# Optimization experiments

Measured on AMD Instinct MI355X. Metric: run time of the kernel, lower is better.

Reference implementation:

```python
import jax, jax.numpy as jnp
import numpy as np

N_NODES = 50000
N_EDGES = 800000
N_GRAPHS = 512
NEG_SLOPE = 0.2  # PyG GATv2Conv default negative_slope

# layer dims: (in_feat, out_channels, heads)
LAYER_DIMS = [(11, 64, 3), (192, 64, 3), (192, 64, 3), (192, 20, 1)]


def setup_inputs() -> dict:
    key = jax.random.key(0)
    ks = jax.random.split(key, 4 + 6 * len(LAYER_DIMS))
    inp = {}
    inp["x"] = jax.random.normal(ks[0], (N_NODES, 11), jnp.float32)
    src = jax.random.randint(ks[1], (N_EDGES,), 0, N_NODES, dtype=jnp.int32)
    dst = jax.random.randint(ks[2], (N_EDGES,), 0, N_NODES, dtype=jnp.int32)
    inp["edge_index"] = jnp.stack([src, dst])
    inp["batch"] = jnp.sort(jax.random.randint(ks[3], (N_NODES,), 0, N_GRAPHS, dtype=jnp.int32))
    ki = 4
    for li, (fi, ch, h) in enumerate(LAYER_DIMS):
        fo = h * ch
        s = 1.0 / np.sqrt(fi)
        inp[f"Wl{li}"] = jax.random.normal(ks[ki + 0], (fo, fi), jnp.float32) * s
        inp[f"bl{li}"] = jnp.zeros((fo,), jnp.float32)
        inp[f"Wr{li}"] = jax.random.normal(ks[ki + 1], (fo, fi), jnp.float32) * s
        inp[f"br{li}"] = jnp.zeros((fo,), jnp.float32)
        inp[f"att{li}"] = jax.random.normal(ks[ki + 2], (h, ch), jnp.float32) * (1.0 / np.sqrt(ch))
        inp[f"b{li}"] = jnp.zeros((fo,), jnp.float32)
        ki += 6
    return inp


def gatv2_layer(x, src, dst, Wl, bl, Wr, br, att, bias, heads, ch):
    """PyG GATv2Conv (concat=True): e = att . leaky_relu(lin_l(x_j)+lin_r(x_i)),
    alpha = softmax over incoming edges of each dst node, out = sum alpha * lin_l(x_j)."""
    N = x.shape[0]
    xl = (x @ Wl.T + bl).reshape(N, heads, ch)  # source transform [N,H,C]
    xr = (x @ Wr.T + br).reshape(N, heads, ch)  # target transform [N,H,C]
    m = xl[src] + xr[dst]                        # [E,H,C] edge-wise gather
    e = jnp.einsum("ehc,hc->eh", jax.nn.leaky_relu(m, NEG_SLOPE), att)  # [E,H]
    emax = jax.ops.segment_max(e, dst, num_segments=N)   # per-dst softmax (stable)
    p = jnp.exp(e - emax[dst])
    denom = jax.ops.segment_sum(p, dst, num_segments=N)
    alpha = p / denom[dst]                        # [E,H]
    out = jax.ops.segment_sum(xl[src] * alpha[..., None], dst, num_segments=N)
    return out.reshape(N, heads * ch) + bias


def reference(x, edge_index, batch,
              Wl0, bl0, Wr0, br0, att0, b0,
              Wl1, bl1, Wr1, br1, att1, b1,
              Wl2, bl2, Wr2, br2, att2, b2,
              Wl3, bl3, Wr3, br3, att3, b3):
    N = x.shape[0]
    loop = jnp.arange(N, dtype=edge_index.dtype)  # add_self_loops=True
    src = jnp.concatenate([edge_index[0], loop])
    dst = jnp.concatenate([edge_index[1], loop])
    h = gatv2_layer(x, src, dst, Wl0, bl0, Wr0, br0, att0, b0, 3, 64)
    h = jax.nn.relu(h)
    h = gatv2_layer(h, src, dst, Wl1, bl1, Wr1, br1, att1, b1, 3, 64)
    h = jax.nn.relu(h)
    h = gatv2_layer(h, src, dst, Wl2, bl2, Wr2, br2, att2, b2, 3, 64)
    h = jax.nn.relu(h)
    h = gatv2_layer(h, src, dst, Wl3, bl3, Wr3, br3, att3, b3, 1, 20)
    # global_add_pool
    return jax.ops.segment_sum(h, batch, num_segments=N_GRAPHS)  # [G, 20]
```

## Files before the change

### kernel.cpp

```cpp
#include <hip/hip_runtime.h>

#define NN 50000
#define NE 800000
#define NT 850000
#define NG 512

typedef __attribute__((ext_vector_type(8))) short bf16x8;
typedef __attribute__((ext_vector_type(4))) float f32x4;


template <int CTRL>
__device__ __forceinline__ float dpp_add(float x) {
  int y = __builtin_amdgcn_update_dpp(0, __float_as_int(x), CTRL, 0xF, 0xF, true);
  return x + __int_as_float(y);
}
template <int CTRL>
__device__ __forceinline__ float dpp_max(float x) {
  int y = __builtin_amdgcn_update_dpp(0, __float_as_int(x), CTRL, 0xF, 0xF, true);
  return fmaxf(x, __int_as_float(y));
}

__device__ __forceinline__ float swz16(float x) {
  return __int_as_float(__builtin_amdgcn_ds_swizzle(__float_as_int(x), 0x401F));
}

__device__ __forceinline__ float rowsum16(float x) {
  x = dpp_add<0xB1>(x);
  x = dpp_add<0x4E>(x);
  x = dpp_add<0x124>(x);
  x = dpp_add<0x128>(x);
  return x;
}
__device__ __forceinline__ float quadsum4(float x) {
  x = dpp_add<0xB1>(x);
  x = dpp_add<0x4E>(x);
  return x;
}
__device__ __forceinline__ float xg_sum(float x) {
  x += swz16(x);
  auto p = __builtin_amdgcn_permlane32_swap(__float_as_uint(x), __float_as_uint(x), false, false);
  return __uint_as_float(p[0]) + __uint_as_float(p[1]);
}
__device__ __forceinline__ float xg_max(float x) {
  x = fmaxf(x, swz16(x));
  auto p = __builtin_amdgcn_permlane32_swap(__float_as_uint(x), __float_as_uint(x), false, false);
  return fmaxf(__uint_as_float(p[0]), __uint_as_float(p[1]));
}
__device__ __forceinline__ float xq_sum(float x) {
  x = dpp_add<0x124>(x);
  x = dpp_add<0x128>(x);
  return xg_sum(x);
}
__device__ __forceinline__ float xq_max(float x) {
  x = dpp_max<0x124>(x);
  x = dpp_max<0x128>(x);
  return xg_max(x);
}

__device__ __forceinline__ float exp2_fast(float x) {
#if __has_builtin(__builtin_amdgcn_exp2f)
  return __builtin_amdgcn_exp2f(x);
#else
  return exp2f(x);
#endif
}

__device__ __forceinline__ float lrelu(float t) { return fmaxf(t, 0.2f * t); }

__device__ __forceinline__ unsigned int f2bf(float f) {
  unsigned int u = __float_as_uint(f);
  u = (u + 0x7FFFu + ((u >> 16) & 1u)) >> 16;
  return u;
}
__device__ __forceinline__ float bf_lo(unsigned int u) { return __uint_as_float(u << 16); }
__device__ __forceinline__ float bf_hi(unsigned int u) { return __uint_as_float(u & 0xFFFF0000u); }
__device__ __forceinline__ float4 bf2f4(uint2 u) {
  return make_float4(bf_lo(u.x), bf_hi(u.x), bf_lo(u.y), bf_hi(u.y));
}

__device__ __forceinline__ void pk_l(float2& d, float2 a, float2 b) {
  asm("v_pk_fma_f32 %0, %1, %2, %0 op_sel_hi:[0,1,1]" : "+v"(d) : "v"(a), "v"(b));
}
__device__ __forceinline__ void pk_h(float2& d, float2 a, float2 b) {
  asm("v_pk_fma_f32 %0, %1, %2, %0 op_sel:[1,0,0]" : "+v"(d) : "v"(a), "v"(b));
}


__global__ void k_hist(const int* __restrict__ dst, int* __restrict__ cnt) {
  int i = blockIdx.x * blockDim.x + threadIdx.x;
  if (i < NT) {
    int d = (i < NE) ? dst[i] : (i - NE);
    atomicAdd(&cnt[d], 1);
  }
}

__global__ __launch_bounds__(1024)
void k_scan(const int* __restrict__ cnt, int* __restrict__ offs) {
  __shared__ int sh[1024];
  int tid = threadIdx.x;
  const int CH = (NN + 1023) / 1024;
  int base = tid * CH;
  int s = 0;
  for (int i = 0; i < CH; ++i) {
    int idx = base + i;
    if (idx < NN) s += cnt[idx];
  }
  sh[tid] = s;
  __syncthreads();
  for (int off = 1; off < 1024; off <<= 1) {
    int t = (tid >= off) ? sh[tid - off] : 0;
    __syncthreads();
    sh[tid] += t;
    __syncthreads();
  }
  int prefix = (tid > 0) ? sh[tid - 1] : 0;
  for (int i = 0; i < CH; ++i) {
    int idx = base + i;
    if (idx < NN) {
      offs[idx] = prefix;
      prefix += cnt[idx];
    }
  }
  if (tid == 1023) offs[NN] = sh[1023];
}

__global__ void k_scatter(const int* __restrict__ src, const int* __restrict__ dst,
                          const int* __restrict__ offs, int* __restrict__ cur,
                          int* __restrict__ srt) {
  int i = blockIdx.x * blockDim.x + threadIdx.x;
  if (i < NT) {
    int s, d;
    if (i < NE) { s = src[i]; d = dst[i]; }
    else        { s = d = i - NE; }
    int pos = offs[d] + atomicAdd(&cur[d], 1);
    srt[pos] = s;
  }
}


__global__ void k_cvtW(const float* __restrict__ a, const float* __restrict__ b,
                       const float* __restrict__ c, const float* __restrict__ d,
                       const float* __restrict__ e, const float* __restrict__ f,
                       unsigned short* __restrict__ out) {
  int i = blockIdx.x * 256 + threadIdx.x;
  if (i >= 155136) return;
  float v;
  if      (i < 36864)  v = a[i];
  else if (i < 73728)  v = b[i - 36864];
  else if (i < 110592) v = c[i - 73728];
  else if (i < 147456) v = d[i - 110592];
  else if (i < 151296) v = e[i - 147456];
  else                 v = f[i - 151296];
  out[i] = (unsigned short)f2bf(v);
}


#define LSTR 200

__global__ __launch_bounds__(256)
void k_gemm_mfma2(const unsigned short* __restrict__ Abf,
                  const unsigned short* __restrict__ W1bf,
                  const unsigned short* __restrict__ W2bf,
                  const float* __restrict__ bias1, const float* __restrict__ bias2,
                  unsigned short* __restrict__ C1, unsigned short* __restrict__ C2,
                  int M, int FO) {
  __shared__ unsigned short Al[64 * LSTR];
  __shared__ unsigned short Bl[2][64 * LSTR];
  int tid = threadIdx.x;
  int mb = blockIdx.x * 64;
  int nb = blockIdx.y * 64;

  {
    int r = tid >> 2, q = tid & 3;
    int ga = min(mb + r, M - 1);
    int gb = min(nb + r, FO - 1);
    const unsigned short* pA = Abf  + (size_t)ga * 192 + q * 48;
    const unsigned short* p1 = W1bf + (size_t)gb * 192 + q * 48;
    const unsigned short* p2 = W2bf + (size_t)gb * 192 + q * 48;
    unsigned short* lA = Al + r * LSTR + q * 48;
    unsigned short* l1 = Bl[0] + r * LSTR + q * 48;
    unsigned short* l2 = Bl[1] + r * LSTR + q * 48;
#pragma unroll
    for (int i = 0; i < 6; ++i) {
      *(bf16x8*)(lA + i * 8) = *(const bf16x8*)(pA + i * 8);
      *(bf16x8*)(l1 + i * 8) = *(const bf16x8*)(p1 + i * 8);
      *(bf16x8*)(l2 + i * 8) = *(const bf16x8*)(p2 + i * 8);
    }
  }
  __syncthreads();

  int l = tid & 63, wid = tid >> 6;
  int wr = (wid >> 1) * 32, wc = (wid & 1) * 32;
  int lr = l & 15, lk = (l >> 4) * 8;

  f32x4 acc[2][2][2];
#pragma unroll
  for (int a = 0; a < 2; ++a)
#pragma unroll
    for (int b = 0; b < 2; ++b)
#pragma unroll
      for (int c = 0; c < 2; ++c) acc[a][b][c] = (f32x4){0.f, 0.f, 0.f, 0.f};

  const unsigned short* pa0 = Al + (wr + 0 + lr) * LSTR + lk;
  const unsigned short* pa1 = Al + (wr + 16 + lr) * LSTR + lk;
  const unsigned short* p10 = Bl[0] + (wc + 0 + lr) * LSTR + lk;
  const unsigned short* p11 = Bl[0] + (wc + 16 + lr) * LSTR + lk;
  const unsigned short* p20 = Bl[1] + (wc + 0 + lr) * LSTR + lk;
  const unsigned short* p21 = Bl[1] + (wc + 16 + lr) * LSTR + lk;
#pragma unroll
  for (int kt = 0; kt < 6; ++kt) {
    bf16x8 a0 = *(const bf16x8*)(pa0 + kt * 32);
    bf16x8 a1 = *(const bf16x8*)(pa1 + kt * 32);
    bf16x8 b10 = *(const bf16x8*)(p10 + kt * 32);
    bf16x8 b11 = *(const bf16x8*)(p11 + kt * 32);
    bf16x8 b20 = *(const bf16x8*)(p20 + kt * 32);
    bf16x8 b21 = *(const bf16x8*)(p21 + kt * 32);
    acc[0][0][0] = __builtin_amdgcn_mfma_f32_16x16x32_bf16(a0, b10, acc[0][0][0], 0, 0, 0);
    acc[0][0][1] = __builtin_amdgcn_mfma_f32_16x16x32_bf16(a0, b11, acc[0][0][1], 0, 0, 0);
    acc[0][1][0] = __builtin_amdgcn_mfma_f32_16x16x32_bf16(a1, b10, acc[0][1][0], 0, 0, 0);
    acc[0][1][1] = __builtin_amdgcn_mfma_f32_16x16x32_bf16(a1, b11, acc[0][1][1], 0, 0, 0);
    acc[1][0][0] = __builtin_amdgcn_mfma_f32_16x16x32_bf16(a0, b20, acc[1][0][0], 0, 0, 0);
    acc[1][0][1] = __builtin_amdgcn_mfma_f32_16x16x32_bf16(a0, b21, acc[1][0][1], 0, 0, 0);
    acc[1][1][0] = __builtin_amdgcn_mfma_f32_16x16x32_bf16(a1, b20, acc[1][1][0], 0, 0, 0);
    acc[1][1][1] = __builtin_amdgcn_mfma_f32_16x16x32_bf16(a1, b21, acc[1][1][1], 0, 0, 0);
  }

  int rb = (l >> 4) * 4;
#pragma unroll
  for (int mt = 0; mt < 2; ++mt) {
    unsigned short* C = mt == 0 ? C1 : C2;
    const float* bias = mt == 0 ? bias1 : bias2;
#pragma unroll
    for (int fn = 0; fn < 2; ++fn) {
      int col = nb + wc + fn * 16 + lr;
      if (col >= FO) continue;
      float bv = bias[col];
#pragma unroll
      for (int fm = 0; fm < 2; ++fm) {
        const f32x4& av = acc[mt][fm][fn];
#pragma unroll
        for (int i = 0; i < 4; ++i) {
          int row = mb + wr + fm * 16 + rb + i;
          if (row < M) C[(size_t)row * FO + col] = (unsigned short)f2bf(av[i] + bv);
        }
      }
    }
  }
}


__global__ __launch_bounds__(256)
void k_gemm_dual(const float* __restrict__ A, int M, int K, int FO,
                 const float* __restrict__ W1, const float* __restrict__ bias1,
                 const float* __restrict__ W2, const float* __restrict__ bias2,
                 unsigned short* __restrict__ C1, unsigned short* __restrict__ C2) {
  constexpr int CT = 16;
  constexpr int BN = CT * 4;
  constexpr int BR = (256 / CT) * 8;
  constexpr int AF4 = BR / 64;
  __shared__ float As[16][BR + 4];
  __shared__ float Bs[2][16][BN + 4];

  int tid = threadIdx.x;
  int tx = tid % CT, ty = tid / CT;
  int mb = blockIdx.x * BR, nb = blockIdx.y * BN;
  int nkt = (K + 15) >> 4;

  float4 sa[AF4], sb1, sb2;

  auto ldrow = [&](const float* P, int row, int lim, int k0, int kq) -> float4 {
    float4 v = make_float4(0.f, 0.f, 0.f, 0.f);
    if (row < lim) {
      float t[4];
#pragma unroll
      for (int i = 0; i < 4; ++i)
        t[i] = (k0 + kq + i < K) ? P[(size_t)row * K + k0 + kq + i] : 0.f;
      v = make_float4(t[0], t[1], t[2], t[3]);
    }
    return v;
  };

  auto loadg = [&](int kt) {
    int k0 = kt * 16;
#pragma unroll
    for (int q = 0; q < AF4; ++q) {
      int f4 = q * 256 + tid;
      sa[q] = ldrow(A, mb + (f4 >> 2), M, k0, (f4 & 3) * 4);
    }
    int row = tid >> 2, kq = (tid & 3) * 4;
    sb1 = ldrow(W1, nb + row, FO, k0, kq);
    sb2 = ldrow(W2, nb + row, FO, k0, kq);
  };

  auto stlds = [&]() {
#pragma unroll
    for (int q = 0; q < AF4; ++q) {
      int f4 = q * 256 + tid;
      int row = f4 >> 2, kq = (f4 & 3) * 4;
      As[kq + 0][row] = sa[q].x; As[kq + 1][row] = sa[q].y;
      As[kq + 2][row] = sa[q].z; As[kq + 3][row] = sa[q].w;
    }
    int row = tid >> 2, kq = (tid & 3) * 4;
    Bs[0][kq + 0][row] = sb1.x; Bs[0][kq + 1][row] = sb1.y;
    Bs[0][kq + 2][row] = sb1.z; Bs[0][kq + 3][row] = sb1.w;
    Bs[1][kq + 0][row] = sb2.x; Bs[1][kq + 1][row] = sb2.y;
    Bs[1][kq + 2][row] = sb2.z; Bs[1][kq + 3][row] = sb2.w;
  };

  float2 c1[8][2], c2[8][2];
#pragma unroll
  for (int r = 0; r < 8; ++r)
#pragma unroll
    for (int j = 0; j < 2; ++j) {
      c1[r][j] = make_float2(0.f, 0.f);
      c2[r][j] = make_float2(0.f, 0.f);
    }

  loadg(0);
  stlds();
  __syncthreads();

  for (int t = 0;;) {
#pragma unroll
    for (int k = 0; k < 16; ++k) {
      float4 av0 = *(const float4*)&As[k][ty * 8 + 0];
      float4 av1 = *(const float4*)&As[k][ty * 8 + 4];
      float4 bv1 = *(const float4*)&Bs[0][k][tx * 4];
      float4 bv2 = *(const float4*)&Bs[1][k][tx * 4];
      float2 f1a = make_float2(bv1.x, bv1.y), f1b = make_float2(bv1.z, bv1.w);
      float2 f2a = make_float2(bv2.x, bv2.y), f2b = make_float2(bv2.z, bv2.w);
      float2 a01 = make_float2(av0.x, av0.y), a23 = make_float2(av0.z, av0.w);
      float2 a45 = make_float2(av1.x, av1.y), a67 = make_float2(av1.z, av1.w);
#define PKROW(rp, a)                                                       \
      pk_l(c1[2 * rp + 0][0], a, f1a); pk_l(c1[2 * rp + 0][1], a, f1b);    \
      pk_h(c1[2 * rp + 1][0], a, f1a); pk_h(c1[2 * rp + 1][1], a, f1b);    \
      pk_l(c2[2 * rp + 0][0], a, f2a); pk_l(c2[2 * rp + 0][1], a, f2b);    \
      pk_h(c2[2 * rp + 1][0], a, f2a); pk_h(c2[2 * rp + 1][1], a, f2b);
      PKROW(0, a01) PKROW(1, a23) PKROW(2, a45) PKROW(3, a67)
#undef PKROW
    }
    if (++t == nkt) break;
    loadg(t);
    __syncthreads();
    stlds();
    __syncthreads();
  }

  int col = nb + tx * 4;
  if (col < FO) {
    float4 bb1 = *(const float4*)&bias1[col];
    float4 bb2 = *(const float4*)&bias2[col];
#pragma unroll
    for (int r = 0; r < 8; ++r) {
      int m = mb + ty * 8 + r;
      if (m >= M) continue;
      uint2 o1, o2;
      o1.x = f2bf(c1[r][0].x + bb1.x) | (f2bf(c1[r][0].y + bb1.y) << 16);
      o1.y = f2bf(c1[r][1].x + bb1.z) | (f2bf(c1[r][1].y + bb1.w) << 16);
      o2.x = f2bf(c2[r][0].x + bb2.x) | (f2bf(c2[r][0].y + bb2.y) << 16);
      o2.y = f2bf(c2[r][1].x + bb2.z) | (f2bf(c2[r][1].y + bb2.w) << 16);
      *(uint2*)&C1[(size_t)m * FO + col] = o1;
      *(uint2*)&C2[(size_t)m * FO + col] = o2;
    }
  }
}


__global__ __launch_bounds__(64)
void k_gat3(const unsigned short* __restrict__ xl, const unsigned short* __restrict__ xr,
            const float* __restrict__ att, const float* __restrict__ bias,
            const int* __restrict__ offs, const int* __restrict__ srt,
            unsigned short* __restrict__ obf, int relu) {
  const float L2E = 1.4426950408889634f;
  int lane = threadIdx.x;
  int grp = lane >> 4, lg = lane & 15;
  int n = blockIdx.x;

  float4 xrv[3], atv[3];
#pragma unroll
  for (int h = 0; h < 3; ++h) {
    xrv[h] = bf2f4(*(const uint2*)(xr + (size_t)n * 192 + h * 64 + lg * 4));
    float4 a = *(const float4*)&att[h * 64 + lg * 4];
    atv[h] = make_float4(a.x * L2E, a.y * L2E, a.z * L2E, a.w * L2E);
  }
  float m[3] = {-1e30f, -1e30f, -1e30f}, d[3] = {0.f, 0.f, 0.f};
  float4 acc[3];
#pragma unroll
  for (int h = 0; h < 3; ++h) acc[h] = make_float4(0.f, 0.f, 0.f, 0.f);

  int e0 = offs[n], e1 = offs[n + 1];
  int nch = (e1 - e0 + 3) >> 2;

  uint2 Rc[3];
  bool vc;
  int j = e0 + grp;
  {
    int jj = min(j, e1 - 1);
    int s = srt[jj];
    const unsigned short* b = xl + (size_t)s * 192 + lg * 4;
    Rc[0] = *(const uint2*)(b);
    Rc[1] = *(const uint2*)(b + 64);
    Rc[2] = *(const uint2*)(b + 128);
    vc = j < e1;
  }
  for (int it = 0; it < nch; ++it) {
    uint2 Rn[3];
    bool vn = false;
    int jn = j + 4;
    if (it + 1 < nch) {
      int jj = min(jn, e1 - 1);
      int s = srt[jj];
      const unsigned short* b = xl + (size_t)s * 192 + lg * 4;
      Rn[0] = *(const uint2*)(b);
      Rn[1] = *(const uint2*)(b + 64);
      Rn[2] = *(const uint2*)(b + 128);
      vn = jn < e1;
    }
    float4 Xc[3];
    Xc[0] = bf2f4(Rc[0]); Xc[1] = bf2f4(Rc[1]); Xc[2] = bf2f4(Rc[2]);
    float part[3];
#pragma unroll
    for (int h = 0; h < 3; ++h) {
      float t = lrelu(Xc[h].x + xrv[h].x);
      float pa = t * atv[h].x;
      t = lrelu(Xc[h].y + xrv[h].y); pa = fmaf(t, atv[h].y, pa);
      t = lrelu(Xc[h].z + xrv[h].z); pa = fmaf(t, atv[h].z, pa);
      t = lrelu(Xc[h].w + xrv[h].w); pa = fmaf(t, atv[h].w, pa);
      part[h] = pa;
    }
#pragma unroll
    for (int h = 0; h < 3; ++h) {
      part[h] = rowsum16(part[h]);
      part[h] = vc ? part[h] : -1e30f;
    }
    float g = fmaxf(fmaxf(part[0] - m[0], part[1] - m[1]), part[2] - m[2]);
    if (__any(g > 11.0f)) {
#pragma unroll
      for (int h = 0; h < 3; ++h) {
        float nm = fmaxf(m[h], part[h]);
        float sc = exp2_fast(m[h] - nm);
        d[h] *= sc;
        acc[h].x *= sc; acc[h].y *= sc; acc[h].z *= sc; acc[h].w *= sc;
        m[h] = nm;
      }
    }
#pragma unroll
    for (int h = 0; h < 3; ++h) {
      float p = vc ? exp2_fast(part[h] - m[h]) : 0.f;
      d[h] += p;
      acc[h].x = fmaf(p, Xc[h].x, acc[h].x);
      acc[h].y = fmaf(p, Xc[h].y, acc[h].y);
      acc[h].z = fmaf(p, Xc[h].z, acc[h].z);
      acc[h].w = fmaf(p, Xc[h].w, acc[h].w);
    }
    Rc[0] = Rn[0]; Rc[1] = Rn[1]; Rc[2] = Rn[2];
    vc = vn; j = jn;
  }

#pragma unroll
  for (int h = 0; h < 3; ++h) {
    float nm = xg_max(m[h]);
    float sc = exp2_fast(m[h] - nm);
    float D = xg_sum(d[h] * sc);
    float A0 = xg_sum(acc[h].x * sc);
    float A1 = xg_sum(acc[h].y * sc);
    float A2 = xg_sum(acc[h].z * sc);
    float A3 = xg_sum(acc[h].w * sc);
    if (grp == 0) {
      float4 bb = *(const float4*)&bias[h * 64 + lg * 4];
      float inv = 1.0f / D;
      float v0 = fmaf(A0, inv, bb.x);
      float v1 = fmaf(A1, inv, bb.y);
      float v2 = fmaf(A2, inv, bb.z);
      float v3 = fmaf(A3, inv, bb.w);
      if (relu) {
        v0 = fmaxf(v0, 0.f); v1 = fmaxf(v1, 0.f);
        v2 = fmaxf(v2, 0.f); v3 = fmaxf(v3, 0.f);
      }
      unsigned int lo = f2bf(v0) | (f2bf(v1) << 16);
      unsigned int hi = f2bf(v2) | (f2bf(v3) << 16);
      *(uint2*)(obf + (size_t)n * 192 + h * 64 + lg * 4) = make_uint2(lo, hi);
    }
  }
}


__global__ __launch_bounds__(64)
void k_gat1(const unsigned short* __restrict__ xl, const unsigned short* __restrict__ xr,
            const float* __restrict__ att, const float* __restrict__ bias,
            const int* __restrict__ offs, const int* __restrict__ srt,
            const int* __restrict__ batch, float* __restrict__ gout) {
  const float L2E = 1.4426950408889634f;
  int lane = threadIdx.x;
  int grp = lane >> 2, lg = lane & 3;
  int n = blockIdx.x;

  float xrv[5], atv[5];
#pragma unroll
  for (int i = 0; i < 5; ++i) {
    xrv[i] = bf_lo(xr[(size_t)n * 20 + lg * 5 + i]);
    atv[i] = att[lg * 5 + i] * L2E;
  }
  float m = -1e30f, d = 0.f, a[5] = {0.f, 0.f, 0.f, 0.f, 0.f};

  int e0 = offs[n], e1 = offs[n + 1];
  int nch = (e1 - e0 + 15) >> 4;

  float Xc[5];
  bool vc;
  int j = e0 + grp;
  {
    int jj = min(j, e1 - 1);
    int s = srt[jj];
    const unsigned short* b = xl + (size_t)s * 20 + lg * 5;
#pragma unroll
    for (int i = 0; i < 5; ++i) Xc[i] = bf_lo(b[i]);
    vc = j < e1;
  }
  for (int it = 0; it < nch; ++it) {
    float Xn[5] = {0.f, 0.f, 0.f, 0.f, 0.f};
    bool vn = false;
    int jn = j + 16;
    if (it + 1 < nch) {
      int jj = min(jn, e1 - 1);
      int s = srt[jj];
      const unsigned short* b = xl + (size_t)s * 20 + lg * 5;
#pragma unroll
      for (int i = 0; i < 5; ++i) Xn[i] = bf_lo(b[i]);
      vn = jn < e1;
    }
    float pa = lrelu(Xc[0] + xrv[0]) * atv[0];
#pragma unroll
    for (int i = 1; i < 5; ++i) pa = fmaf(lrelu(Xc[i] + xrv[i]), atv[i], pa);
    pa = quadsum4(pa);
    pa = vc ? pa : -1e30f;
    if (__any(pa - m > 11.0f)) {
      float nm = fmaxf(m, pa);
      float sc = exp2_fast(m - nm);
      d *= sc;
#pragma unroll
      for (int i = 0; i < 5; ++i) a[i] *= sc;
      m = nm;
    }
    float p = vc ? exp2_fast(pa - m) : 0.f;
    d += p;
#pragma unroll
    for (int i = 0; i < 5; ++i) a[i] = fmaf(p, Xc[i], a[i]);
#pragma unroll
    for (int i = 0; i < 5; ++i) Xc[i] = Xn[i];
    vc = vn; j = jn;
  }

  float nm = xq_max(m);
  float sc = exp2_fast(m - nm);
  float D = xq_sum(d * sc);
  float A[5];
#pragma unroll
  for (int i = 0; i < 5; ++i) A[i] = xq_sum(a[i] * sc);
  if (grp == 0) {
    int gb = batch[n] * 20 + lg * 5;
    float inv = 1.0f / D;
#pragma unroll
    for (int i = 0; i < 5; ++i)
      atomicAdd(&gout[gb + i], fmaf(A[i], inv, bias[lg * 5 + i]));
  }
}


extern "C" void kernel_launch(void* const* d_in, const int* in_sizes, int n_in,
                              void* d_out, int out_size, void* d_ws, size_t ws_size,
                              hipStream_t stream) {
  const float* x = (const float*)d_in[0];
  const int* src = (const int*)d_in[1];
  const int* dst = src + NE;
  const int* batch = (const int*)d_in[2];
  const float *Wl[4], *bl[4], *Wr[4], *br[4], *att[4], *bb[4];
  for (int li = 0; li < 4; ++li) {
    Wl[li]  = (const float*)d_in[3 + li * 6 + 0];
    bl[li]  = (const float*)d_in[3 + li * 6 + 1];
    Wr[li]  = (const float*)d_in[3 + li * 6 + 2];
    br[li]  = (const float*)d_in[3 + li * 6 + 3];
    att[li] = (const float*)d_in[3 + li * 6 + 4];
    bb[li]  = (const float*)d_in[3 + li * 6 + 5];
  }

  char* p = (char*)d_ws;
  auto alloc = [&](size_t bytes) {
    char* r = p;
    p += (bytes + 255) & ~(size_t)255;
    return r;
  };
  unsigned short* xlbf = (unsigned short*)alloc((size_t)NN * 192 * 2);
  unsigned short* xrbf = (unsigned short*)alloc((size_t)NN * 192 * 2);
  unsigned short* hbf  = (unsigned short*)alloc((size_t)NN * 192 * 2);
  unsigned short* wb   = (unsigned short*)alloc((size_t)155136 * 2);
  int* srt   = (int*)alloc((size_t)NT * 4);
  int* offs  = (int*)alloc((size_t)(NN + 1) * 4);
  int* cnt   = (int*)alloc((size_t)NN * 4);
  int* cur   = (int*)alloc((size_t)NN * 4);

  hipMemsetAsync(cnt, 0, (size_t)NN * 4, stream);
  hipMemsetAsync(cur, 0, (size_t)NN * 4, stream);
  hipMemsetAsync(d_out, 0, (size_t)NG * 20 * 4, stream);

  k_hist<<<(NT + 255) / 256, 256, 0, stream>>>(dst, cnt);
  k_scan<<<1, 1024, 0, stream>>>(cnt, offs);
  k_scatter<<<(NT + 255) / 256, 256, 0, stream>>>(src, dst, offs, cur, srt);
  k_cvtW<<<(155136 + 255) / 256, 256, 0, stream>>>(Wl[1], Wr[1], Wl[2], Wr[2], Wl[3], Wr[3], wb);

  {
    dim3 g((NN + 127) / 128, 3);
    k_gemm_dual<<<g, 256, 0, stream>>>(x, NN, 11, 192, Wl[0], bl[0], Wr[0], br[0], xlbf, xrbf);
    k_gat3<<<NN, 64, 0, stream>>>(xlbf, xrbf, att[0], bb[0], offs, srt, hbf, 1);
  }
  {
    dim3 gm((NN + 63) / 64, 3);
    k_gemm_mfma2<<<gm, 256, 0, stream>>>(hbf, wb + 0, wb + 36864, bl[1], br[1], xlbf, xrbf, NN, 192);
    k_gat3<<<NN, 64, 0, stream>>>(xlbf, xrbf, att[1], bb[1], offs, srt, hbf, 1);
    k_gemm_mfma2<<<gm, 256, 0, stream>>>(hbf, wb + 73728, wb + 110592, bl[2], br[2], xlbf, xrbf, NN, 192);
    k_gat3<<<NN, 64, 0, stream>>>(xlbf, xrbf, att[2], bb[2], offs, srt, hbf, 1);
  }
  {
    dim3 gm((NN + 63) / 64, 1);
    k_gemm_mfma2<<<gm, 256, 0, stream>>>(hbf, wb + 147456, wb + 151296, bl[3], br[3], xlbf, xrbf, NN, 20);
    k_gat1<<<NN, 64, 0, stream>>>(xlbf, xrbf, att[3], bb[3], offs, srt, batch, (float*)d_out);
  }
}
```

Measured before the change: 584.0 us.

## Parallelize CSR offset scan across blocks and pack four nodes per GAT block

Replaces the single-block serial-chunk prefix scan over node degrees with a three-kernel multi-block scan: per-block scan, a tiny serial pass over block sums, then a fixup add. It also changes the GAT aggregation kernels from one 64-thread block per node to 256-thread blocks handling four nodes each, with a bounds check. The scan change removes a long single-workgroup serial phase at the cost of two extra launches. The block packing cuts block count and scheduling overhead.

```diff
diff --git a/kernel.cpp b/kernel.cpp
--- a/kernel.cpp
+++ b/kernel.cpp
@@ -4,6 +4,7 @@
 #define NE 800000
 #define NT 850000
 #define NG 512
+#define NSB 49
 
 typedef __attribute__((ext_vector_type(8))) short bf16x8;
 typedef __attribute__((ext_vector_type(4))) float f32x4;
@@ -95,17 +96,12 @@
 }
 
 __global__ __launch_bounds__(1024)
-void k_scan(const int* __restrict__ cnt, int* __restrict__ offs) {
+void k_scanA(const int* __restrict__ cnt, int* __restrict__ offs, int* __restrict__ bsum) {
   __shared__ int sh[1024];
   int tid = threadIdx.x;
-  const int CH = (NN + 1023) / 1024;
-  int base = tid * CH;
-  int s = 0;
-  for (int i = 0; i < CH; ++i) {
-    int idx = base + i;
-    if (idx < NN) s += cnt[idx];
-  }
-  sh[tid] = s;
+  int idx = blockIdx.x * 1024 + tid;
+  int v = (idx < NN) ? cnt[idx] : 0;
+  sh[tid] = v;
   __syncthreads();
   for (int off = 1; off < 1024; off <<= 1) {
     int t = (tid >= off) ? sh[tid - off] : 0;
@@ -113,15 +109,25 @@
     sh[tid] += t;
     __syncthreads();
   }
-  int prefix = (tid > 0) ? sh[tid - 1] : 0;
-  for (int i = 0; i < CH; ++i) {
-    int idx = base + i;
-    if (idx < NN) {
-      offs[idx] = prefix;
-      prefix += cnt[idx];
-    }
-  }
-  if (tid == 1023) offs[NN] = sh[1023];
+  if (idx < NN) offs[idx] = sh[tid] - v;
+  if (tid == 1023) bsum[blockIdx.x] = sh[1023];
+}
+
+__global__ void k_scanB(int* __restrict__ bsum, int* __restrict__ offs) {
+  int tot = 0;
+#pragma unroll 7
+  for (int i = 0; i < NSB; ++i) {
+    int v = bsum[i];
+    bsum[i] = tot;
+    tot += v;
+  }
+  offs[NN] = tot;
+}
+
+__global__ __launch_bounds__(1024)
+void k_scanC(int* __restrict__ offs, const int* __restrict__ bsum) {
+  int idx = blockIdx.x * 1024 + threadIdx.x;
+  if (idx < NN) offs[idx] += bsum[blockIdx.x];
 }
 
 __global__ void k_scatter(const int* __restrict__ src, const int* __restrict__ dst,
@@ -366,15 +372,16 @@
 }
 
 
-__global__ __launch_bounds__(64)
+__global__ __launch_bounds__(256)
 void k_gat3(const unsigned short* __restrict__ xl, const unsigned short* __restrict__ xr,
             const float* __restrict__ att, const float* __restrict__ bias,
             const int* __restrict__ offs, const int* __restrict__ srt,
             unsigned short* __restrict__ obf, int relu) {
   const float L2E = 1.4426950408889634f;
-  int lane = threadIdx.x;
+  int lane = threadIdx.x & 63;
   int grp = lane >> 4, lg = lane & 15;
-  int n = blockIdx.x;
+  int n = blockIdx.x * 4 + (threadIdx.x >> 6);
+  if (n >= NN) return;
 
   float4 xrv[3], atv[3];
 #pragma unroll
@@ -485,15 +492,16 @@
 }
 
 
-__global__ __launch_bounds__(64)
+__global__ __launch_bounds__(256)
 void k_gat1(const unsigned short* __restrict__ xl, const unsigned short* __restrict__ xr,
             const float* __restrict__ att, const float* __restrict__ bias,
             const int* __restrict__ offs, const int* __restrict__ srt,
             const int* __restrict__ batch, float* __restrict__ gout) {
   const float L2E = 1.4426950408889634f;
-  int lane = threadIdx.x;
+  int lane = threadIdx.x & 63;
   int grp = lane >> 2, lg = lane & 3;
-  int n = blockIdx.x;
+  int n = blockIdx.x * 4 + (threadIdx.x >> 6);
+  if (n >= NN) return;
 
   float xrv[5], atv[5];
 #pragma unroll
@@ -598,31 +606,34 @@
   int* offs  = (int*)alloc((size_t)(NN + 1) * 4);
   int* cnt   = (int*)alloc((size_t)NN * 4);
   int* cur   = (int*)alloc((size_t)NN * 4);
+  int* bsum  = (int*)alloc((size_t)NSB * 4);
 
   hipMemsetAsync(cnt, 0, (size_t)NN * 4, stream);
   hipMemsetAsync(cur, 0, (size_t)NN * 4, stream);
   hipMemsetAsync(d_out, 0, (size_t)NG * 20 * 4, stream);
 
   k_hist<<<(NT + 255) / 256, 256, 0, stream>>>(dst, cnt);
-  k_scan<<<1, 1024, 0, stream>>>(cnt, offs);
+  k_scanA<<<NSB, 1024, 0, stream>>>(cnt, offs, bsum);
+  k_scanB<<<1, 1, 0, stream>>>(bsum, offs);
+  k_scanC<<<NSB, 1024, 0, stream>>>(offs, bsum);
   k_scatter<<<(NT + 255) / 256, 256, 0, stream>>>(src, dst, offs, cur, srt);
   k_cvtW<<<(155136 + 255) / 256, 256, 0, stream>>>(Wl[1], Wr[1], Wl[2], Wr[2], Wl[3], Wr[3], wb);
 
   {
     dim3 g((NN + 127) / 128, 3);
     k_gemm_dual<<<g, 256, 0, stream>>>(x, NN, 11, 192, Wl[0], bl[0], Wr[0], br[0], xlbf, xrbf);
-    k_gat3<<<NN, 64, 0, stream>>>(xlbf, xrbf, att[0], bb[0], offs, srt, hbf, 1);
+    k_gat3<<<(NN + 3) / 4, 256, 0, stream>>>(xlbf, xrbf, att[0], bb[0], offs, srt, hbf, 1);
   }
   {
     dim3 gm((NN + 63) / 64, 3);
     k_gemm_mfma2<<<gm, 256, 0, stream>>>(hbf, wb + 0, wb + 36864, bl[1], br[1], xlbf, xrbf, NN, 192);
-    k_gat3<<<NN, 64, 0, stream>>>(xlbf, xrbf, att[1], bb[1], offs, srt, hbf, 1);
+    k_gat3<<<(NN + 3) / 4, 256, 0, stream>>>(xlbf, xrbf, att[1], bb[1], offs, srt, hbf, 1);
     k_gemm_mfma2<<<gm, 256, 0, stream>>>(hbf, wb + 73728, wb + 110592, bl[2], br[2], xlbf, xrbf, NN, 192);
-    k_gat3<<<NN, 64, 0, stream>>>(xlbf, xrbf, att[2], bb[2], offs, srt, hbf, 1);
+    k_gat3<<<(NN + 3) / 4, 256, 0, stream>>>(xlbf, xrbf, att[2], bb[2], offs, srt, hbf, 1);
   }
   {
     dim3 gm((NN + 63) / 64, 1);
     k_gemm_mfma2<<<gm, 256, 0, stream>>>(hbf, wb + 147456, wb + 151296, bl[3], br[3], xlbf, xrbf, NN, 20);
-    k_gat1<<<NN, 64, 0, stream>>>(xlbf, xrbf, att[3], bb[3], offs, srt, batch, (float*)d_out);
-  }
-}
+    k_gat1<<<(NN + 3) / 4, 256, 0, stream>>>(xlbf, xrbf, att[3], bb[3], offs, srt, batch, (float*)d_out);
+  }
+}
```

After: 550.2 us. 1.06x faster.
